# Optimization experiments

Hardware: AMD Instinct MI355X
Metric: run time of the kernel (lower is better)

The kernel has to match this reference:

```python
import jax, jax.numpy as jnp
import numpy as np

C = 256
CQK = C // 8  # query/key channels from Conv2d(in_dim, in_dim//8, 1)


def _cross_attn(x, y, qw, qb, kw, kb, vw, vb, gamma):
    # x, y: [B, C, H, W]; 1x1 convs are channel matmuls
    B, Cc, H, W = x.shape
    N = H * W
    xf = x.reshape(B, Cc, N)
    yf = y.reshape(B, Cc, N)
    q = jnp.einsum('oc,bcn->bno', qw, xf) + qb  # [B, N, CQK]
    k = jnp.einsum('oc,bcn->bon', kw, yf) + kb[:, None]  # [B, CQK, N]
    energy = jnp.einsum('bnc,bcm->bnm', q, k)  # [B, N, N]
    attn = jax.nn.softmax(energy, axis=2)
    v = jnp.einsum('oc,bcn->bon', vw, yf) + vb[:, None]  # [B, C, N]
    out = jnp.einsum('bcm,bnm->bcn', v, attn)  # value @ attention^T
    out = out.reshape(B, Cc, H, W)
    return gamma * out + x


def setup_inputs() -> dict:
    key = jax.random.key(0)
    ks = jax.random.split(key, 16)
    B, H, W = 4, 64, 64
    s = 1.0 / np.sqrt(C)
    d = {
        'x': jax.random.normal(ks[0], (B, C, H, W), jnp.float32),
        'y': jax.random.normal(ks[1], (B, C, H, W), jnp.float32),
        'z': jax.random.normal(ks[2], (B, C, H, W), jnp.float32),
        'q1_w': jax.random.normal(ks[3], (CQK, C), jnp.float32) * s,
        'q1_b': jax.random.normal(ks[4], (CQK,), jnp.float32) * s,
        'k1_w': jax.random.normal(ks[5], (CQK, C), jnp.float32) * s,
        'k1_b': jax.random.normal(ks[6], (CQK,), jnp.float32) * s,
        'v1_w': jax.random.normal(ks[7], (C, C), jnp.float32) * s,
        'v1_b': jax.random.normal(ks[8], (C,), jnp.float32) * s,
        'gamma1': jax.random.normal(ks[9], (1,), jnp.float32) * 0.1,
        'q2_w': jax.random.normal(ks[10], (CQK, C), jnp.float32) * s,
        'q2_b': jax.random.normal(ks[11], (CQK,), jnp.float32) * s,
        'k2_w': jax.random.normal(ks[12], (CQK, C), jnp.float32) * s,
        'k2_b': jax.random.normal(ks[13], (CQK,), jnp.float32) * s,
        'v2_w': jax.random.normal(ks[14], (C, C), jnp.float32) * s,
        'v2_b': jax.random.normal(ks[15], (C,), jnp.float32) * s,
        'gamma2': jax.random.normal(jax.random.fold_in(key, 99), (1,), jnp.float32) * 0.1,
    }
    return d


def reference(x, y, z, q1_w, q1_b, k1_w, k1_b, v1_w, v1_b, gamma1,
              q2_w, q2_b, k2_w, k2_b, v2_w, v2_b, gamma2):
    out1 = _cross_attn(x, y, q1_w, q1_b, k1_w, k1_b, v1_w, v1_b, gamma1)
    out2 = _cross_attn(out1, z, q2_w, q2_b, k2_w, k2_b, v2_w, v2_b, gamma2)
    return out2
```

## Files before the change

### kernel.cpp

```cpp
#include <hip/hip_runtime.h>
#include <hip/hip_bf16.h>

#define NSEQ 4096
#define CDIM 256
#define CQKD 32
#define LOG2E 1.4426950408889634f

typedef float v4f __attribute__((ext_vector_type(4)));
typedef float v16f __attribute__((ext_vector_type(16)));
typedef short v8s __attribute__((ext_vector_type(8)));
typedef unsigned long long u64;

__device__ __forceinline__ float exp2_(float x) {
#if __has_builtin(__builtin_amdgcn_exp2f)
  return __builtin_amdgcn_exp2f(x);
#else
  float r;
  __asm__("v_exp_f32 %0, %1" : "=v"(r) : "v"(x));
  return r;
#endif
}

__device__ __forceinline__ unsigned short f2bf(float x) {
  unsigned u = __builtin_bit_cast(unsigned, x);
  unsigned r = (u + 0x7FFFu + ((u >> 16) & 1u)) >> 16;
  return (unsigned short)r;
}
__device__ __forceinline__ float bf2f(unsigned short s) {
  unsigned u = ((unsigned)s) << 16;
  return __builtin_bit_cast(float, u);
}
__device__ __forceinline__ unsigned int pack_bf16(float a, float b) {
#if __has_builtin(__builtin_amdgcn_cvt_pk_bf16_f32)
  typedef __bf16 v2bf __attribute__((ext_vector_type(2)));
  v2bf r = __builtin_amdgcn_cvt_pk_bf16_f32(a, b);
  return __builtin_bit_cast(unsigned int, r);
#else
  return ((unsigned)f2bf(b) << 16) | (unsigned)f2bf(a);
#endif
}

__device__ __forceinline__ unsigned char f2e4m3(float x) {
  unsigned u = __builtin_bit_cast(unsigned, x);
  unsigned s = (u >> 24) & 0x80u;
  unsigned au = u & 0x7fffffffu;
  if (au > 0x43e00000u) return (unsigned char)(s | 0x7eu);
  if (au < 0x3c800000u) {
    float ax = __builtin_bit_cast(float, au);
    int q = (int)(ax * 512.0f + 0.5f);
    if (q > 7) q = 7;
    return (unsigned char)(s | (unsigned)q);
  }
  int e = (int)((au >> 23) & 0xffu) - 127 + 7;
  unsigned m = au & 0x7fffffu;
  unsigned mr = m + 0x7ffffu + ((m >> 20) & 1u);
  if (mr >= 0x800000u) { mr -= 0x800000u; e += 1; if (e >= 16) return (unsigned char)(s | 0x7e); }
  return (unsigned char)(s | ((unsigned)e << 3) | (mr >> 20));
}
__device__ __forceinline__ unsigned int pack4_fp8(float a, float b, float c, float d) {
#if __has_builtin(__builtin_amdgcn_cvt_pk_fp8_f32)
  int v = 0;
  v = __builtin_amdgcn_cvt_pk_fp8_f32(a, b, v, false);
  v = __builtin_amdgcn_cvt_pk_fp8_f32(c, d, v, true);
  return (unsigned int)v;
#else
  return (unsigned)f2e4m3(a) | ((unsigned)f2e4m3(b) << 8) |
         ((unsigned)f2e4m3(c) << 16) | ((unsigned)f2e4m3(d) << 24);
#endif
}

__device__ __forceinline__ void barrier_lds() {
  __asm__ __volatile__("s_waitcnt lgkmcnt(0)\n\ts_barrier" ::: "memory");
}

__global__ __launch_bounds__(256) void convw_kernel(
    const float* __restrict__ q1w, const float* __restrict__ k1w,
    const float* __restrict__ k2w, const float* __restrict__ q2w,
    const float* __restrict__ v1w, const float* __restrict__ v2w,
    unsigned short* __restrict__ W) {
  const int s = blockIdx.x * 256 + threadIdx.x;
  const float* src;
  int o, ch0;
  size_t obase;
  float scale = 1.0f;
  if (s < 3072) {
    const int wsel = s >> 10, r = s & 1023;
    src = wsel == 0 ? q1w : (wsel == 1 ? k1w : k2w);
    const int ot = r >> 9, cb = (r >> 6) & 7, lane = r & 63;
    o = ot * 16 + (lane & 15);
    ch0 = cb * 32 + ((lane >> 4) & 3) * 8;
    obase = (size_t)wsel * 8192 + (size_t)r * 8;
  } else if (s < 19456) {
    const int s2 = s - 3072, which = s2 >> 13, r = s2 & 8191;
    src = which == 0 ? v1w : v2w;
    const int ot = r >> 9, cb = (r >> 6) & 7, lane = r & 63;
    o = ot * 16 + (lane & 15);
    ch0 = cb * 32 + ((lane >> 4) & 3) * 8;
    obase = 32768 + (size_t)which * 65536 + (size_t)r * 8;
  } else {
    const int r = s - 19456;
    src = q2w;
    const int lane = r & 63;
    o = lane & 31;
    ch0 = (r >> 6) * 16 + (lane >> 5) * 8;
    obase = 24576 + (size_t)r * 8;
    scale = LOG2E;
  }
#pragma unroll
  for (int j = 0; j < 8; ++j)
    W[obase + j] = f2bf(src[o * CDIM + ch0 + j] * scale);
}

__global__ __launch_bounds__(256) void prep_kernel(
    const float* __restrict__ x, const float* __restrict__ y,
    const float* __restrict__ z, const unsigned short* __restrict__ Wbf,
    const float* __restrict__ q1b, const float* __restrict__ k1b,
    const float* __restrict__ k2b, const float* __restrict__ v1b,
    const float* __restrict__ v2b, unsigned short* __restrict__ Q1,
    unsigned short* __restrict__ K1, unsigned short* __restrict__ K2,
    unsigned char* __restrict__ V1, unsigned char* __restrict__ V2) {
  __shared__ unsigned short t[256][72];
  __shared__ unsigned short Kt[64][40];
  const int src = blockIdx.z;
  const float* in = src == 0 ? x : (src == 1 ? y : z);
  const int b = blockIdx.y;
  const int n0 = blockIdx.x * 64;
  const int tid = threadIdx.x, lane = tid & 63, w = tid >> 6;
  const int quad = lane >> 4, r15 = lane & 15, l31 = lane & 31, lh = lane >> 5;
  const float* ip = in + (size_t)(b * CDIM) * NSEQ + n0;
  {
    const int chb = tid >> 4, c4 = (tid & 15) * 4;
#pragma unroll
    for (int p = 0; p < 16; ++p) {
      const int ch = p * 16 + chb;
      float4 v = *(const float4*)(ip + (size_t)ch * NSEQ + c4);
      uint2 pk;
      pk.x = pack_bf16(v.x, v.y);
      pk.y = pack_bf16(v.z, v.w);
      *(uint2*)&t[ch][c4] = pk;
    }
  }
  __syncthreads();
  v8s af[8];
#pragma unroll
  for (int cb = 0; cb < 8; ++cb) {
    union { unsigned short e[8]; v8s v; } u;
#pragma unroll
    for (int j = 0; j < 8; ++j) u.e[j] = t[cb * 32 + quad * 8 + j][w * 16 + r15];
    af[cb] = u.v;
  }
  const int nt = blockIdx.x * 4 + w;
  const unsigned short* Wqk = Wbf + src * 8192;
  v4f a0 = {0.f, 0.f, 0.f, 0.f}, a1 = a0;
#pragma unroll
  for (int cb = 0; cb < 8; ++cb) {
    v8s b0 = *(const v8s*)(Wqk + (size_t)cb * 512 + lane * 8);
    v8s b1 = *(const v8s*)(Wqk + (size_t)(8 + cb) * 512 + lane * 8);
    a0 = __builtin_amdgcn_mfma_f32_16x16x32_bf16(af[cb], b0, a0, 0, 0, 0);
    a1 = __builtin_amdgcn_mfma_f32_16x16x32_bf16(af[cb], b1, a1, 0, 0, 0);
  }
  if (src == 0) {
#pragma unroll
    for (int r = 0; r < 4; ++r) {
      Q1[((size_t)b * NSEQ + nt * 16 + quad * 4 + r) * CQKD + r15] =
          f2bf((a0[r] + q1b[r15]) * LOG2E);
      Q1[((size_t)b * NSEQ + nt * 16 + quad * 4 + r) * CQKD + 16 + r15] =
          f2bf((a1[r] + q1b[16 + r15]) * LOG2E);
    }
    return;
  }
  const float* kbias = src == 1 ? k1b : k2b;
#pragma unroll
  for (int r = 0; r < 4; ++r) {
    Kt[w * 16 + quad * 4 + r][r15] = f2bf(a0[r] + kbias[r15]);
    Kt[w * 16 + quad * 4 + r][16 + r15] = f2bf(a1[r] + kbias[16 + r15]);
  }
  const unsigned short* Wv = Wbf + 32768 + (src - 1) * 65536;
  const float* vbias = src == 1 ? v1b : v2b;
  v4f vacc[16];
#pragma unroll
  for (int ot = 0; ot < 16; ++ot) vacc[ot] = (v4f){0.f, 0.f, 0.f, 0.f};
#pragma unroll
  for (int cb = 0; cb < 8; ++cb) {
    const v8s afc = af[cb];
#pragma unroll
    for (int ot = 0; ot < 16; ++ot) {
      v8s bf = *(const v8s*)(Wv + (size_t)(ot * 8 + cb) * 512 + lane * 8);
      vacc[ot] = __builtin_amdgcn_mfma_f32_16x16x32_bf16(afc, bf, vacc[ot], 0, 0, 0);
    }
  }
  __syncthreads();
  unsigned char* Vt8 = (unsigned char*)t;
#pragma unroll
  for (int ot = 0; ot < 16; ++ot) {
    const int ch = ot * 16 + r15;
    const float bv = vbias[ch];
    *(unsigned int*)&Vt8[(size_t)ch * 72 + w * 16 + quad * 4] =
        pack4_fp8(vacc[ot][0] + bv, vacc[ot][1] + bv, vacc[ot][2] + bv, vacc[ot][3] + bv);
  }
  {
    unsigned short* Kout = (src == 1 ? K1 : K2) + (size_t)b * (NSEQ / 16) * 512;
    *(v8s*)(Kout + ((size_t)nt * 64 + lane) * 8) = *(const v8s*)&Kt[w * 16 + r15][quad * 8];
  }
  __syncthreads();
  unsigned char* Vout = (src == 1 ? V1 : V2) + (size_t)b * (NSEQ / 16) * 8 * 512;
#pragma unroll
  for (int chb = 0; chb < 8; ++chb)
    *(u64*)(Vout + (((size_t)nt * 8 + chb) * 64 + lane) * 8) =
        *(const u64*)&Vt8[(size_t)(chb * 32 + l31) * 72 + w * 16 + lh * 8];
}


__device__ __forceinline__ void max_pass(
    const unsigned short* __restrict__ Kp, const v8s qf[4], int w, int lane,
    float (*lbuf)[64], float m[4]) {
  const v4f vzero4 = {0.f, 0.f, 0.f, 0.f};
  const int r15 = lane & 15;
  const unsigned short* Kl = Kp + (size_t)w * 512 + lane * 8;
  v8s kA = *(const v8s*)(Kl);
#pragma unroll
  for (int qt = 0; qt < 4; ++qt) m[qt] = -3.0e38f;
  for (int kt = 0; kt < 32; ++kt) {
    v8s kB = *(const v8s*)(Kl + (size_t)((kt + 1) & 31) * 4096);
#pragma unroll
    for (int qt = 0; qt < 4; ++qt) {
      v4f st = __builtin_amdgcn_mfma_f32_16x16x32_bf16(kA, qf[qt], vzero4, 0, 0, 0);
      m[qt] = fmaxf(m[qt], fmaxf(fmaxf(st[0], st[1]), fmaxf(st[2], st[3])));
    }
    kA = kB;
  }
#pragma unroll
  for (int qt = 0; qt < 4; ++qt) {
    m[qt] = fmaxf(m[qt], __shfl_xor(m[qt], 16));
    m[qt] = fmaxf(m[qt], __shfl_xor(m[qt], 32));
  }
  if (lane < 16) {
#pragma unroll
    for (int qt = 0; qt < 4; ++qt) lbuf[w][qt * 16 + lane] = m[qt];
  }
  __syncthreads();
#pragma unroll
  for (int qt = 0; qt < 4; ++qt) {
    float mm = lbuf[0][qt * 16 + r15];
#pragma unroll
    for (int ww = 1; ww < 8; ++ww) mm = fmaxf(mm, lbuf[ww][qt * 16 + r15]);
    m[qt] = mm;
  }
  __syncthreads();
}

__device__ __forceinline__ void attn_tile(
    const unsigned short* __restrict__ Kl, const unsigned char* __restrict__ Vl,
    unsigned char* __restrict__ P, const v8s qf[4], const float m[4], int w, int lane,
    int pbuf, int tn, const v8s kfu, const u64* vfu, v8s& kfn, u64* vfn,
    v16f acc[2], float lsum[4]) {
  const v4f vzero4 = {0.f, 0.f, 0.f, 0.f};
  const int quad = (lane >> 4) & 3, r15 = lane & 15;
  const int l31 = lane & 31, lh = lane >> 5;
  kfn = *(const v8s*)(Kl + (size_t)tn * 4096);
#pragma unroll
  for (int s = 0; s < 8; ++s)
    vfn[s] = *(const u64*)(Vl + (size_t)tn * 32768 + s * 4096);
  unsigned char* pw = P + pbuf * 8704 + w * 16 + quad * 4;
#pragma unroll
  for (int qt = 0; qt < 4; ++qt) {
    v4f st = __builtin_amdgcn_mfma_f32_16x16x32_bf16(kfu, qf[qt], vzero4, 0, 0, 0);
    float e0 = exp2_(st[0] - m[qt]), e1 = exp2_(st[1] - m[qt]);
    float e2 = exp2_(st[2] - m[qt]), e3 = exp2_(st[3] - m[qt]);
    lsum[qt] += (e0 + e1) + (e2 + e3);
    *(unsigned int*)(pw + (size_t)(qt * 16 + r15) * 136) = pack4_fp8(e0, e1, e2, e3);
  }
  barrier_lds();
  const unsigned char* pb = P + pbuf * 8704;
#pragma unroll
  for (int s = 0; s < 8; ++s) {
    long pf0 = (long)*(const u64*)(pb + (size_t)l31 * 136 + s * 16 + lh * 8);
    long pf1 = (long)*(const u64*)(pb + (size_t)(32 + l31) * 136 + s * 16 + lh * 8);
    acc[0] = __builtin_amdgcn_mfma_f32_32x32x16_fp8_fp8((long)vfu[s], pf0, acc[0], 0, 0, 0);
    acc[1] = __builtin_amdgcn_mfma_f32_32x32x16_fp8_fp8((long)vfu[s], pf1, acc[1], 0, 0, 0);
  }
}

__device__ __forceinline__ void attn_loop(
    const unsigned short* __restrict__ Kp, const unsigned char* __restrict__ Vp,
    unsigned char* __restrict__ P, const v8s qf[4], const float m[4], int w, int lane,
    v16f acc[2], float lsum[4]) {
  const unsigned short* Kl = Kp + (size_t)w * 512 + lane * 8;
  const unsigned char* Vl = Vp + (size_t)w * 512 + lane * 8;
  v8s kA, kB;
  u64 vA[8], vB[8];
  kA = *(const v8s*)(Kl);
#pragma unroll
  for (int s = 0; s < 8; ++s) vA[s] = *(const u64*)(Vl + (size_t)s * 4096);
  for (int kt = 0; kt < 32; kt += 2) {
    attn_tile(Kl, Vl, P, qf, m, w, lane, 0, (kt + 1) & 31, kA, vA, kB, vB, acc, lsum);
    attn_tile(Kl, Vl, P, qf, m, w, lane, 1, (kt + 2) & 31, kB, vB, kA, vA, acc, lsum);
  }
}

__global__ __launch_bounds__(512, 2) void fused_attn_kernel(
    const unsigned short* __restrict__ Q1g, const unsigned short* __restrict__ K1g,
    const unsigned char* __restrict__ V1g, const unsigned short* __restrict__ K2g,
    const unsigned char* __restrict__ V2g, const unsigned short* __restrict__ W2g,
    const float* __restrict__ x, const float* __restrict__ q2b,
    const float* __restrict__ g1p, const float* __restrict__ g2p,
    float* __restrict__ outp) {
  __shared__ __align__(16) unsigned char P[2 * 8704];
  __shared__ __align__(16) unsigned short out1T[64 * 264];
  __shared__ __align__(16) unsigned short q2s[64 * 32];
  __shared__ float lbuf[8][64];

  const int tid = threadIdx.x;
  const int lane = tid & 63;
  const int w = tid >> 6;
  const int quad = lane >> 4;
  const int r15 = lane & 15;
  const int l31 = lane & 31, lh = lane >> 5;
  const int b = blockIdx.x & 3;
  const int n0 = (blockIdx.x >> 2) * 64;

  const float g1 = g1p[0];
  const float g2 = g2p[0];

  const unsigned short* Qp  = Q1g + (size_t)b * NSEQ * CQKD;
  const unsigned short* K1p = K1g + (size_t)b * (NSEQ / 16) * 512;
  const unsigned short* K2p = K2g + (size_t)b * (NSEQ / 16) * 512;
  const unsigned char* V1p  = V1g + (size_t)b * (NSEQ / 16) * 8 * 512;
  const unsigned char* V2p  = V2g + (size_t)b * (NSEQ / 16) * 8 * 512;

  v8s qf[4];
#pragma unroll
  for (int qt = 0; qt < 4; ++qt)
    qf[qt] = *(const v8s*)(Qp + (n0 + qt * 16 + r15) * CQKD + quad * 8);

  v16f acc[2];
  float lsum[4] = {0.f, 0.f, 0.f, 0.f};
  float m[4];
  acc[0] = (v16f)(0.f); acc[1] = (v16f)(0.f);

  max_pass(K1p, qf, w, lane, lbuf, m);
  attn_loop(K1p, V1p, P, qf, m, w, lane, acc, lsum);
#pragma unroll
  for (int qt = 0; qt < 4; ++qt) {
    lsum[qt] += __shfl_xor(lsum[qt], 16);
    lsum[qt] += __shfl_xor(lsum[qt], 32);
  }
  __syncthreads();
  if (lane < 16) {
#pragma unroll
    for (int qt = 0; qt < 4; ++qt) lbuf[w][qt * 16 + lane] = lsum[qt];
  }
  __syncthreads();
  float rinv[2];
#pragma unroll
  for (int qh = 0; qh < 2; ++qh) {
    const int q = qh * 32 + l31;
    float d = 0.f;
#pragma unroll
    for (int ww = 0; ww < 8; ++ww) d += lbuf[ww][q];
    rinv[qh] = 1.0f / d;
  }
#pragma unroll
  for (int qh = 0; qh < 2; ++qh) {
    const int q = qh * 32 + l31;
#pragma unroll
    for (int rg = 0; rg < 4; ++rg) {
      const int c = w * 32 + 8 * rg + 4 * lh;
      float o0 = g1 * (acc[qh][rg * 4 + 0] * rinv[qh]) + x[((size_t)b * CDIM + c + 0) * NSEQ + n0 + q];
      float o1 = g1 * (acc[qh][rg * 4 + 1] * rinv[qh]) + x[((size_t)b * CDIM + c + 1) * NSEQ + n0 + q];
      float o2 = g1 * (acc[qh][rg * 4 + 2] * rinv[qh]) + x[((size_t)b * CDIM + c + 2) * NSEQ + n0 + q];
      float o3 = g1 * (acc[qh][rg * 4 + 3] * rinv[qh]) + x[((size_t)b * CDIM + c + 3) * NSEQ + n0 + q];
      uint2 pk;
      pk.x = pack_bf16(o0, o1);
      pk.y = pack_bf16(o2, o3);
      *(uint2*)(out1T + (size_t)q * 264 + c) = pk;
    }
  }
  __syncthreads();

  if (w < 2) {
    const int qh = w;
    v16f qacc = (v16f)(0.f);
#pragma unroll
    for (int s = 0; s < 16; ++s) {
      v8s af = *(const v8s*)(W2g + (size_t)(s * 64 + lane) * 8);
      v8s bf = *(const v8s*)(out1T + (size_t)(qh * 32 + l31) * 264 + s * 16 + lh * 8);
      qacc = __builtin_amdgcn_mfma_f32_32x32x16_bf16(af, bf, qacc, 0, 0, 0);
    }
#pragma unroll
    for (int rg = 0; rg < 4; ++rg) {
      const int o = 8 * rg + 4 * lh;
      uint2 pk;
      pk.x = pack_bf16(qacc[rg * 4 + 0] + q2b[o + 0] * LOG2E, qacc[rg * 4 + 1] + q2b[o + 1] * LOG2E);
      pk.y = pack_bf16(qacc[rg * 4 + 2] + q2b[o + 2] * LOG2E, qacc[rg * 4 + 3] + q2b[o + 3] * LOG2E);
      *(uint2*)(q2s + (size_t)(qh * 32 + l31) * 32 + o) = pk;
    }
  }
  __syncthreads();

#pragma unroll
  for (int qt = 0; qt < 4; ++qt)
    qf[qt] = *(const v8s*)(q2s + (qt * 16 + r15) * 32 + quad * 8);
  acc[0] = (v16f)(0.f); acc[1] = (v16f)(0.f);
#pragma unroll
  for (int qt = 0; qt < 4; ++qt) lsum[qt] = 0.f;
  max_pass(K2p, qf, w, lane, lbuf, m);
  attn_loop(K2p, V2p, P, qf, m, w, lane, acc, lsum);
#pragma unroll
  for (int qt = 0; qt < 4; ++qt) {
    lsum[qt] += __shfl_xor(lsum[qt], 16);
    lsum[qt] += __shfl_xor(lsum[qt], 32);
  }
  __syncthreads();
  if (lane < 16) {
#pragma unroll
    for (int qt = 0; qt < 4; ++qt) lbuf[w][qt * 16 + lane] = lsum[qt];
  }
  __syncthreads();
#pragma unroll
  for (int qh = 0; qh < 2; ++qh) {
    const int q = qh * 32 + l31;
    float d = 0.f;
#pragma unroll
    for (int ww = 0; ww < 8; ++ww) d += lbuf[ww][q];
    rinv[qh] = 1.0f / d;
  }
#pragma unroll
  for (int qh = 0; qh < 2; ++qh) {
    const int q = qh * 32 + l31;
#pragma unroll
    for (int rg = 0; rg < 4; ++rg) {
      const int c = w * 32 + 8 * rg + 4 * lh;
#pragma unroll
      for (int i = 0; i < 4; ++i) {
        float res = bf2f(out1T[(size_t)q * 264 + c + i]);
        outp[((size_t)b * CDIM + c + i) * NSEQ + n0 + q] =
            g2 * (acc[qh][rg * 4 + i] * rinv[qh]) + res;
      }
    }
  }
}

extern "C" void kernel_launch(void* const* d_in, const int* in_sizes, int n_in,
                              void* d_out, int out_size, void* d_ws, size_t ws_size,
                              hipStream_t stream) {
  const float* x   = (const float*)d_in[0];
  const float* y   = (const float*)d_in[1];
  const float* z   = (const float*)d_in[2];
  const float* q1w = (const float*)d_in[3];
  const float* q1b = (const float*)d_in[4];
  const float* k1w = (const float*)d_in[5];
  const float* k1b = (const float*)d_in[6];
  const float* v1w = (const float*)d_in[7];
  const float* v1b = (const float*)d_in[8];
  const float* g1  = (const float*)d_in[9];
  const float* q2w = (const float*)d_in[10];
  const float* q2b = (const float*)d_in[11];
  const float* k2w = (const float*)d_in[12];
  const float* k2b = (const float*)d_in[13];
  const float* v2w = (const float*)d_in[14];
  const float* v2b = (const float*)d_in[15];
  const float* g2  = (const float*)d_in[16];
  char* ws = (char*)d_ws;
  unsigned short* Wbf = (unsigned short*)(ws);
  unsigned short* Q1  = (unsigned short*)(ws + 327680);
  unsigned short* K1  = (unsigned short*)(ws + 1376256);
  unsigned short* K2  = (unsigned short*)(ws + 2424832);
  unsigned char*  V1  = (unsigned char*)(ws + 3473408);
  unsigned char*  V2  = (unsigned char*)(ws + 7667712);
  float* outp = (float*)d_out;

  convw_kernel<<<dim3(80), 256, 0, stream>>>(q1w, k1w, k2w, q2w, v1w, v2w, Wbf);
  prep_kernel<<<dim3(64, 4, 3), 256, 0, stream>>>(x, y, z, Wbf, q1b, k1b, k2b, v1b,
                                                  v2b, Q1, K1, K2, V1, V2);
  fused_attn_kernel<<<dim3(256), 512, 0, stream>>>(Q1, K1, V1, K2, V2, Wbf + 24576, x,
                                                   q2b, g1, g2, outp);
}
```

Baseline: 222.1 us.

## Replace two-pass softmax with online split-K attention and shuffle-based P exchange

Drops the separate max pass over K and switches each attention stage to online softmax, rescaling lazily only when the running max grows by more than a threshold. The key dimension is split across four waves per query group of 32, and partial accumulators are merged at the end through LDS with the max/sum correction. The probability tile is rebuilt in registers with cross-lane shuffles instead of an LDS write, barrier and read. Each wave now holds eight 32x32 fp32 accumulators plus prefetched V fragments. That adds a lot of register pressure under the 512x2 launch bounds and a serial three-round LDS reduction.

```diff
diff --git a/kernel.cpp b/kernel.cpp
--- a/kernel.cpp
+++ b/kernel.cpp
@@ -67,10 +67,6 @@
   return (unsigned)f2e4m3(a) | ((unsigned)f2e4m3(b) << 8) |
          ((unsigned)f2e4m3(c) << 16) | ((unsigned)f2e4m3(d) << 24);
 #endif
-}
-
-__device__ __forceinline__ void barrier_lds() {
-  __asm__ __volatile__("s_waitcnt lgkmcnt(0)\n\ts_barrier" ::: "memory");
 }
 
 __global__ __launch_bounds__(256) void convw_kernel(
@@ -211,91 +207,67 @@
 }
 
 
-__device__ __forceinline__ void max_pass(
-    const unsigned short* __restrict__ Kp, const v8s qf[4], int w, int lane,
-    float (*lbuf)[64], float m[4]) {
-  const v4f vzero4 = {0.f, 0.f, 0.f, 0.f};
-  const int r15 = lane & 15;
-  const unsigned short* Kl = Kp + (size_t)w * 512 + lane * 8;
-  v8s kA = *(const v8s*)(Kl);
-#pragma unroll
-  for (int qt = 0; qt < 4; ++qt) m[qt] = -3.0e38f;
-  for (int kt = 0; kt < 32; ++kt) {
-    v8s kB = *(const v8s*)(Kl + (size_t)((kt + 1) & 31) * 4096);
-#pragma unroll
-    for (int qt = 0; qt < 4; ++qt) {
-      v4f st = __builtin_amdgcn_mfma_f32_16x16x32_bf16(kA, qf[qt], vzero4, 0, 0, 0);
-      m[qt] = fmaxf(m[qt], fmaxf(fmaxf(st[0], st[1]), fmaxf(st[2], st[3])));
-    }
-    kA = kB;
-  }
-#pragma unroll
-  for (int qt = 0; qt < 4; ++qt) {
-    m[qt] = fmaxf(m[qt], __shfl_xor(m[qt], 16));
-    m[qt] = fmaxf(m[qt], __shfl_xor(m[qt], 32));
-  }
-  if (lane < 16) {
-#pragma unroll
-    for (int qt = 0; qt < 4; ++qt) lbuf[w][qt * 16 + lane] = m[qt];
-  }
-  __syncthreads();
-#pragma unroll
-  for (int qt = 0; qt < 4; ++qt) {
-    float mm = lbuf[0][qt * 16 + r15];
-#pragma unroll
-    for (int ww = 1; ww < 8; ++ww) mm = fmaxf(mm, lbuf[ww][qt * 16 + r15]);
-    m[qt] = mm;
-  }
-  __syncthreads();
-}
-
-__device__ __forceinline__ void attn_tile(
-    const unsigned short* __restrict__ Kl, const unsigned char* __restrict__ Vl,
-    unsigned char* __restrict__ P, const v8s qf[4], const float m[4], int w, int lane,
-    int pbuf, int tn, const v8s kfu, const u64* vfu, v8s& kfn, u64* vfn,
-    v16f acc[2], float lsum[4]) {
-  const v4f vzero4 = {0.f, 0.f, 0.f, 0.f};
-  const int quad = (lane >> 4) & 3, r15 = lane & 15;
+__device__ __forceinline__ void attn_ks(
+    const unsigned short* __restrict__ Kp, const unsigned char* __restrict__ Vp,
+    const v8s qfA, const v8s qfB, int ks, int lane,
+    v16f acc[8], float& m, float& lsum) {
   const int l31 = lane & 31, lh = lane >> 5;
-  kfn = *(const v8s*)(Kl + (size_t)tn * 4096);
-#pragma unroll
-  for (int s = 0; s < 8; ++s)
-    vfn[s] = *(const u64*)(Vl + (size_t)tn * 32768 + s * 4096);
-  unsigned char* pw = P + pbuf * 8704 + w * 16 + quad * 4;
-#pragma unroll
-  for (int qt = 0; qt < 4; ++qt) {
-    v4f st = __builtin_amdgcn_mfma_f32_16x16x32_bf16(kfu, qf[qt], vzero4, 0, 0, 0);
-    float e0 = exp2_(st[0] - m[qt]), e1 = exp2_(st[1] - m[qt]);
-    float e2 = exp2_(st[2] - m[qt]), e3 = exp2_(st[3] - m[qt]);
-    lsum[qt] += (e0 + e1) + (e2 + e3);
-    *(unsigned int*)(pw + (size_t)(qt * 16 + r15) * 136) = pack4_fp8(e0, e1, e2, e3);
-  }
-  barrier_lds();
-  const unsigned char* pb = P + pbuf * 8704;
-#pragma unroll
-  for (int s = 0; s < 8; ++s) {
-    long pf0 = (long)*(const u64*)(pb + (size_t)l31 * 136 + s * 16 + lh * 8);
-    long pf1 = (long)*(const u64*)(pb + (size_t)(32 + l31) * 136 + s * 16 + lh * 8);
-    acc[0] = __builtin_amdgcn_mfma_f32_32x32x16_fp8_fp8((long)vfu[s], pf0, acc[0], 0, 0, 0);
-    acc[1] = __builtin_amdgcn_mfma_f32_32x32x16_fp8_fp8((long)vfu[s], pf1, acc[1], 0, 0, 0);
-  }
-}
-
-__device__ __forceinline__ void attn_loop(
-    const unsigned short* __restrict__ Kp, const unsigned char* __restrict__ Vp,
-    unsigned char* __restrict__ P, const v8s qf[4], const float m[4], int w, int lane,
-    v16f acc[2], float lsum[4]) {
-  const unsigned short* Kl = Kp + (size_t)w * 512 + lane * 8;
-  const unsigned char* Vl = Vp + (size_t)w * 512 + lane * 8;
-  v8s kA, kB;
-  u64 vA[8], vB[8];
-  kA = *(const v8s*)(Kl);
-#pragma unroll
-  for (int s = 0; s < 8; ++s) vA[s] = *(const u64*)(Vl + (size_t)s * 4096);
-  for (int kt = 0; kt < 32; kt += 2) {
-    attn_tile(Kl, Vl, P, qf, m, w, lane, 0, (kt + 1) & 31, kA, vA, kB, vB, acc, lsum);
-    attn_tile(Kl, Vl, P, qf, m, w, lane, 1, (kt + 2) & 31, kB, vB, kA, vA, acc, lsum);
-  }
+  const char* Kb = (const char*)Kp + (size_t)ks * 65536 + (size_t)(l31 >> 4) * 1024 +
+                   (size_t)lh * 256 + (size_t)(l31 & 15) * 16;
+  const char* Vb = (const char*)Vp + (size_t)ks * 262144 + (size_t)lane * 8;
+  m = -3.0e38f;
+  lsum = 0.f;
+  v8s kA = *(const v8s*)(Kb);
+  v8s kB = *(const v8s*)(Kb + 512);
+#pragma unroll 1
+  for (int t = 0; t < 32; ++t) {
+    u64 v0[8], v1[8];
+#pragma unroll
+    for (int s = 0; s < 8; ++s) v0[s] = *(const u64*)(Vb + (size_t)t * 8192 + s * 512);
+#pragma unroll
+    for (int s = 0; s < 8; ++s) v1[s] = *(const u64*)(Vb + (size_t)t * 8192 + 4096 + s * 512);
+    v16f st = (v16f)(0.f);
+    st = __builtin_amdgcn_mfma_f32_32x32x16_bf16(kA, qfA, st, 0, 0, 0);
+    st = __builtin_amdgcn_mfma_f32_32x32x16_bf16(kB, qfB, st, 0, 0, 0);
+    if (t < 31) {
+      kA = *(const v8s*)(Kb + (size_t)(t + 1) * 2048);
+      kB = *(const v8s*)(Kb + (size_t)(t + 1) * 2048 + 512);
+    }
+    float tmax = st[0];
+#pragma unroll
+    for (int g = 1; g < 16; ++g) tmax = fmaxf(tmax, st[g]);
+    tmax = fmaxf(tmax, __shfl_xor(tmax, 32));
+    if (__any(tmax > m + 8.0f)) {
+      float mn = fmaxf(m, tmax);
+      float sc = exp2_(m - mn);
+#pragma unroll
+      for (int s = 0; s < 8; ++s) acc[s] *= sc;
+      lsum *= sc;
+      m = mn;
+    }
+    float esum = 0.f;
+    unsigned pw[4];
+#pragma unroll
+    for (int h = 0; h < 4; ++h) {
+      float e0 = exp2_(st[4 * h + 0] - m), e1 = exp2_(st[4 * h + 1] - m);
+      float e2 = exp2_(st[4 * h + 2] - m), e3 = exp2_(st[4 * h + 3] - m);
+      esum += (e0 + e1) + (e2 + e3);
+      pw[h] = pack4_fp8(e0, e1, e2, e3);
+    }
+    lsum += esum;
+    unsigned X0 = (unsigned)__shfl_xor((int)pw[0], 32);
+    unsigned X1 = (unsigned)__shfl_xor((int)pw[1], 32);
+    unsigned X2 = (unsigned)__shfl_xor((int)pw[2], 32);
+    unsigned X3 = (unsigned)__shfl_xor((int)pw[3], 32);
+    u64 fA = lh ? ((u64)X1 | ((u64)pw[1] << 32)) : ((u64)pw[0] | ((u64)X0 << 32));
+    u64 fB = lh ? ((u64)X3 | ((u64)pw[3] << 32)) : ((u64)pw[2] | ((u64)X2 << 32));
+#pragma unroll
+    for (int s = 0; s < 8; ++s) {
+      acc[s] = __builtin_amdgcn_mfma_f32_32x32x16_fp8_fp8((long)v0[s], (long)fA, acc[s], 0, 0, 0);
+      acc[s] = __builtin_amdgcn_mfma_f32_32x32x16_fp8_fp8((long)v1[s], (long)fB, acc[s], 0, 0, 0);
+    }
+  }
+  lsum += __shfl_xor(lsum, 32);
 }
 
 __global__ __launch_bounds__(512, 2) void fused_attn_kernel(
@@ -305,19 +277,21 @@
     const float* __restrict__ x, const float* __restrict__ q2b,
     const float* __restrict__ g1p, const float* __restrict__ g2p,
     float* __restrict__ outp) {
-  __shared__ __align__(16) unsigned char P[2 * 8704];
+  __shared__ float cb[2][256][32];
   __shared__ __align__(16) unsigned short out1T[64 * 264];
   __shared__ __align__(16) unsigned short q2s[64 * 32];
-  __shared__ float lbuf[8][64];
+  __shared__ float mbuf[8][32];
+  __shared__ float sbuf[8][32];
 
   const int tid = threadIdx.x;
   const int lane = tid & 63;
   const int w = tid >> 6;
-  const int quad = lane >> 4;
-  const int r15 = lane & 15;
+  const int qg = w >> 2;
+  const int ks = w & 3;
   const int l31 = lane & 31, lh = lane >> 5;
   const int b = blockIdx.x & 3;
   const int n0 = (blockIdx.x >> 2) * 64;
+  const int q = qg * 32 + l31;
 
   const float g1 = g1p[0];
   const float g2 = g2p[0];
@@ -328,52 +302,61 @@
   const unsigned char* V1p  = V1g + (size_t)b * (NSEQ / 16) * 8 * 512;
   const unsigned char* V2p  = V2g + (size_t)b * (NSEQ / 16) * 8 * 512;
 
-  v8s qf[4];
-#pragma unroll
-  for (int qt = 0; qt < 4; ++qt)
-    qf[qt] = *(const v8s*)(Qp + (n0 + qt * 16 + r15) * CQKD + quad * 8);
-
-  v16f acc[2];
-  float lsum[4] = {0.f, 0.f, 0.f, 0.f};
-  float m[4];
-  acc[0] = (v16f)(0.f); acc[1] = (v16f)(0.f);
-
-  max_pass(K1p, qf, w, lane, lbuf, m);
-  attn_loop(K1p, V1p, P, qf, m, w, lane, acc, lsum);
-#pragma unroll
-  for (int qt = 0; qt < 4; ++qt) {
-    lsum[qt] += __shfl_xor(lsum[qt], 16);
-    lsum[qt] += __shfl_xor(lsum[qt], 32);
-  }
-  __syncthreads();
-  if (lane < 16) {
-#pragma unroll
-    for (int qt = 0; qt < 4; ++qt) lbuf[w][qt * 16 + lane] = lsum[qt];
-  }
-  __syncthreads();
-  float rinv[2];
-#pragma unroll
-  for (int qh = 0; qh < 2; ++qh) {
-    const int q = qh * 32 + l31;
-    float d = 0.f;
-#pragma unroll
-    for (int ww = 0; ww < 8; ++ww) d += lbuf[ww][q];
-    rinv[qh] = 1.0f / d;
-  }
-#pragma unroll
-  for (int qh = 0; qh < 2; ++qh) {
-    const int q = qh * 32 + l31;
-#pragma unroll
-    for (int rg = 0; rg < 4; ++rg) {
-      const int c = w * 32 + 8 * rg + 4 * lh;
-      float o0 = g1 * (acc[qh][rg * 4 + 0] * rinv[qh]) + x[((size_t)b * CDIM + c + 0) * NSEQ + n0 + q];
-      float o1 = g1 * (acc[qh][rg * 4 + 1] * rinv[qh]) + x[((size_t)b * CDIM + c + 1) * NSEQ + n0 + q];
-      float o2 = g1 * (acc[qh][rg * 4 + 2] * rinv[qh]) + x[((size_t)b * CDIM + c + 2) * NSEQ + n0 + q];
-      float o3 = g1 * (acc[qh][rg * 4 + 3] * rinv[qh]) + x[((size_t)b * CDIM + c + 3) * NSEQ + n0 + q];
-      uint2 pk;
-      pk.x = pack_bf16(o0, o1);
-      pk.y = pack_bf16(o2, o3);
-      *(uint2*)(out1T + (size_t)q * 264 + c) = pk;
+  v16f acc[8];
+#pragma unroll
+  for (int s = 0; s < 8; ++s) acc[s] = (v16f)(0.f);
+  float m, lsum;
+
+  {
+    v8s qfA = *(const v8s*)(Qp + (size_t)(n0 + q) * CQKD + lh * 8);
+    v8s qfB = *(const v8s*)(Qp + (size_t)(n0 + q) * CQKD + 16 + lh * 8);
+    attn_ks(K1p, V1p, qfA, qfB, ks, lane, acc, m, lsum);
+  }
+  mbuf[w][l31] = m;
+  sbuf[w][l31] = lsum;
+  __syncthreads();
+  float mstar = mbuf[qg * 4 + 0][l31];
+#pragma unroll
+  for (int k = 1; k < 4; ++k) mstar = fmaxf(mstar, mbuf[qg * 4 + k][l31]);
+  float L = 0.f;
+#pragma unroll
+  for (int k = 0; k < 4; ++k) L += sbuf[qg * 4 + k][l31] * exp2_(mbuf[qg * 4 + k][l31] - mstar);
+  {
+    float sc = exp2_(m - mstar);
+#pragma unroll
+    for (int s = 0; s < 8; ++s) acc[s] *= sc;
+  }
+#pragma unroll 1
+  for (int r = 1; r < 4; ++r) {
+    if (ks == r) {
+#pragma unroll
+      for (int s = 0; s < 8; ++s)
+#pragma unroll
+        for (int g = 0; g < 16; ++g)
+          cb[qg][s * 32 + (g & 3) + 8 * (g >> 2) + 4 * lh][l31] = acc[s][g];
+    }
+    __syncthreads();
+    if (ks == 0) {
+#pragma unroll
+      for (int s = 0; s < 8; ++s)
+#pragma unroll
+        for (int g = 0; g < 16; ++g)
+          acc[s][g] += cb[qg][s * 32 + (g & 3) + 8 * (g >> 2) + 4 * lh][l31];
+    }
+    __syncthreads();
+  }
+  if (ks == 0) {
+    const float rinv = 1.0f / L;
+    const float* xb = x + (size_t)b * CDIM * NSEQ + n0 + q;
+#pragma unroll
+    for (int s = 0; s < 8; ++s) {
+#pragma unroll
+      for (int j = 0; j < 8; ++j) {
+        const int ch = s * 32 + ((2 * j) & 3) + 8 * (j >> 1) + 4 * lh;
+        float o0 = g1 * (acc[s][2 * j] * rinv) + xb[(size_t)ch * NSEQ];
+        float o1 = g1 * (acc[s][2 * j + 1] * rinv) + xb[(size_t)(ch + 1) * NSEQ];
+        *(unsigned*)(&out1T[(size_t)q * 264 + ch]) = pack_bf16(o0, o1);
+      }
     }
   }
   __syncthreads();
@@ -399,43 +382,57 @@
   __syncthreads();
 
 #pragma unroll
-  for (int qt = 0; qt < 4; ++qt)
-    qf[qt] = *(const v8s*)(q2s + (qt * 16 + r15) * 32 + quad * 8);
-  acc[0] = (v16f)(0.f); acc[1] = (v16f)(0.f);
-#pragma unroll
-  for (int qt = 0; qt < 4; ++qt) lsum[qt] = 0.f;
-  max_pass(K2p, qf, w, lane, lbuf, m);
-  attn_loop(K2p, V2p, P, qf, m, w, lane, acc, lsum);
-#pragma unroll
-  for (int qt = 0; qt < 4; ++qt) {
-    lsum[qt] += __shfl_xor(lsum[qt], 16);
-    lsum[qt] += __shfl_xor(lsum[qt], 32);
-  }
-  __syncthreads();
-  if (lane < 16) {
-#pragma unroll
-    for (int qt = 0; qt < 4; ++qt) lbuf[w][qt * 16 + lane] = lsum[qt];
-  }
-  __syncthreads();
-#pragma unroll
-  for (int qh = 0; qh < 2; ++qh) {
-    const int q = qh * 32 + l31;
-    float d = 0.f;
-#pragma unroll
-    for (int ww = 0; ww < 8; ++ww) d += lbuf[ww][q];
-    rinv[qh] = 1.0f / d;
-  }
-#pragma unroll
-  for (int qh = 0; qh < 2; ++qh) {
-    const int q = qh * 32 + l31;
-#pragma unroll
-    for (int rg = 0; rg < 4; ++rg) {
-      const int c = w * 32 + 8 * rg + 4 * lh;
-#pragma unroll
-      for (int i = 0; i < 4; ++i) {
-        float res = bf2f(out1T[(size_t)q * 264 + c + i]);
-        outp[((size_t)b * CDIM + c + i) * NSEQ + n0 + q] =
-            g2 * (acc[qh][rg * 4 + i] * rinv[qh]) + res;
+  for (int s = 0; s < 8; ++s) acc[s] = (v16f)(0.f);
+  {
+    v8s qfA = *(const v8s*)(q2s + (size_t)q * 32 + lh * 8);
+    v8s qfB = *(const v8s*)(q2s + (size_t)q * 32 + 16 + lh * 8);
+    attn_ks(K2p, V2p, qfA, qfB, ks, lane, acc, m, lsum);
+  }
+  mbuf[w][l31] = m;
+  sbuf[w][l31] = lsum;
+  __syncthreads();
+  mstar = mbuf[qg * 4 + 0][l31];
+#pragma unroll
+  for (int k = 1; k < 4; ++k) mstar = fmaxf(mstar, mbuf[qg * 4 + k][l31]);
+  L = 0.f;
+#pragma unroll
+  for (int k = 0; k < 4; ++k) L += sbuf[qg * 4 + k][l31] * exp2_(mbuf[qg * 4 + k][l31] - mstar);
+  {
+    float sc = exp2_(m - mstar);
+#pragma unroll
+    for (int s = 0; s < 8; ++s) acc[s] *= sc;
+  }
+#pragma unroll 1
+  for (int r = 1; r < 4; ++r) {
+    if (ks == r) {
+#pragma unroll
+      for (int s = 0; s < 8; ++s)
+#pragma unroll
+        for (int g = 0; g < 16; ++g)
+          cb[qg][s * 32 + (g & 3) + 8 * (g >> 2) + 4 * lh][l31] = acc[s][g];
+    }
+    __syncthreads();
+    if (ks == 0) {
+#pragma unroll
+      for (int s = 0; s < 8; ++s)
+#pragma unroll
+        for (int g = 0; g < 16; ++g)
+          acc[s][g] += cb[qg][s * 32 + (g & 3) + 8 * (g >> 2) + 4 * lh][l31];
+    }
+    __syncthreads();
+  }
+  if (ks == 0) {
+    const float rinv = 1.0f / L;
+    float* ob = outp + (size_t)b * CDIM * NSEQ + n0 + q;
+#pragma unroll
+    for (int s = 0; s < 8; ++s) {
+#pragma unroll
+      for (int j = 0; j < 8; ++j) {
+        const int ch = s * 32 + ((2 * j) & 3) + 8 * (j >> 1) + 4 * lh;
+        float r0 = bf2f(out1T[(size_t)q * 264 + ch]);
+        float r1 = bf2f(out1T[(size_t)q * 264 + ch + 1]);
+        ob[(size_t)ch * NSEQ] = g2 * (acc[s][2 * j] * rinv) + r0;
+        ob[(size_t)(ch + 1) * NSEQ] = g2 * (acc[s][2 * j + 1] * rinv) + r1;
       }
     }
   }
```

After: 248.7 us. 12.0% more time.

## Software-pipeline attention loop: overlap next tile's scores with current PV MFMAs

Applied to the files above, without the earlier changes.

Restructures the attention inner loop so each step computes the QK scores and fp8 P tile for tile t+1 while running the PV MFMAs on tile t from the other P buffer. This cuts one barrier per tile and lets exp/score work overlap the matrix work. V loads are issued after the PV MFMAs, and the max pass gets deeper K prefetch with unroll 2. Register pressure rises and the prefetch distances have to line up with the double-buffered P.

```diff
diff --git a/kernel.cpp b/kernel.cpp
--- a/kernel.cpp
+++ b/kernel.cpp
@@ -218,16 +218,19 @@
   const int r15 = lane & 15;
   const unsigned short* Kl = Kp + (size_t)w * 512 + lane * 8;
   v8s kA = *(const v8s*)(Kl);
+  v8s kB = *(const v8s*)(Kl + 4096);
 #pragma unroll
   for (int qt = 0; qt < 4; ++qt) m[qt] = -3.0e38f;
+#pragma unroll 2
   for (int kt = 0; kt < 32; ++kt) {
-    v8s kB = *(const v8s*)(Kl + (size_t)((kt + 1) & 31) * 4096);
+    v8s kC = *(const v8s*)(Kl + (size_t)((kt + 2) & 31) * 4096);
 #pragma unroll
     for (int qt = 0; qt < 4; ++qt) {
       v4f st = __builtin_amdgcn_mfma_f32_16x16x32_bf16(kA, qf[qt], vzero4, 0, 0, 0);
       m[qt] = fmaxf(m[qt], fmaxf(fmaxf(st[0], st[1]), fmaxf(st[2], st[3])));
     }
     kA = kB;
+    kB = kC;
   }
 #pragma unroll
   for (int qt = 0; qt < 4; ++qt) {
@@ -249,42 +252,46 @@
   __syncthreads();
 }
 
-__device__ __forceinline__ void attn_tile(
+__device__ __forceinline__ void attn_step(
     const unsigned short* __restrict__ Kl, const unsigned char* __restrict__ Vl,
     unsigned char* __restrict__ P, const v8s qf[4], const float m[4], int w, int lane,
-    int pbuf, int tn, const v8s kfu, const u64* vfu, v8s& kfn, u64* vfn,
+    bool doS, int pbufW, int pbufR, int tpre, const v8s kS, v8s& kOut, u64 vUse[8],
     v16f acc[2], float lsum[4]) {
   const v4f vzero4 = {0.f, 0.f, 0.f, 0.f};
   const int quad = (lane >> 4) & 3, r15 = lane & 15;
   const int l31 = lane & 31, lh = lane >> 5;
-  kfn = *(const v8s*)(Kl + (size_t)tn * 4096);
-#pragma unroll
-  for (int s = 0; s < 8; ++s)
-    vfn[s] = *(const u64*)(Vl + (size_t)tn * 32768 + s * 4096);
-  unsigned char* pw = P + pbuf * 8704 + w * 16 + quad * 4;
-#pragma unroll
-  for (int qt = 0; qt < 4; ++qt) {
-    v4f st = __builtin_amdgcn_mfma_f32_16x16x32_bf16(kfu, qf[qt], vzero4, 0, 0, 0);
-    float e0 = exp2_(st[0] - m[qt]), e1 = exp2_(st[1] - m[qt]);
-    float e2 = exp2_(st[2] - m[qt]), e3 = exp2_(st[3] - m[qt]);
-    lsum[qt] += (e0 + e1) + (e2 + e3);
-    *(unsigned int*)(pw + (size_t)(qt * 16 + r15) * 136) = pack4_fp8(e0, e1, e2, e3);
-  }
-  barrier_lds();
-  const unsigned char* pb = P + pbuf * 8704;
+  kOut = *(const v8s*)(Kl + (size_t)tpre * 4096);
+  if (doS) {
+    unsigned char* pw = P + pbufW * 8704 + w * 16 + quad * 4;
+#pragma unroll
+    for (int qt = 0; qt < 4; ++qt) {
+      v4f st = __builtin_amdgcn_mfma_f32_16x16x32_bf16(kS, qf[qt], vzero4, 0, 0, 0);
+      float e0 = exp2_(st[0] - m[qt]), e1 = exp2_(st[1] - m[qt]);
+      float e2 = exp2_(st[2] - m[qt]), e3 = exp2_(st[3] - m[qt]);
+      lsum[qt] += (e0 + e1) + (e2 + e3);
+      *(unsigned int*)(pw + (size_t)(qt * 16 + r15) * 136) = pack4_fp8(e0, e1, e2, e3);
+    }
+  }
+  const unsigned char* pb = P + pbufR * 8704;
 #pragma unroll
   for (int s = 0; s < 8; ++s) {
     long pf0 = (long)*(const u64*)(pb + (size_t)l31 * 136 + s * 16 + lh * 8);
     long pf1 = (long)*(const u64*)(pb + (size_t)(32 + l31) * 136 + s * 16 + lh * 8);
-    acc[0] = __builtin_amdgcn_mfma_f32_32x32x16_fp8_fp8((long)vfu[s], pf0, acc[0], 0, 0, 0);
-    acc[1] = __builtin_amdgcn_mfma_f32_32x32x16_fp8_fp8((long)vfu[s], pf1, acc[1], 0, 0, 0);
-  }
+    acc[0] = __builtin_amdgcn_mfma_f32_32x32x16_fp8_fp8((long)vUse[s], pf0, acc[0], 0, 0, 0);
+    acc[1] = __builtin_amdgcn_mfma_f32_32x32x16_fp8_fp8((long)vUse[s], pf1, acc[1], 0, 0, 0);
+  }
+#pragma unroll
+  for (int s = 0; s < 8; ++s)
+    vUse[s] = *(const u64*)(Vl + (size_t)tpre * 32768 + s * 4096);
+  barrier_lds();
 }
 
 __device__ __forceinline__ void attn_loop(
     const unsigned short* __restrict__ Kp, const unsigned char* __restrict__ Vp,
     unsigned char* __restrict__ P, const v8s qf[4], const float m[4], int w, int lane,
     v16f acc[2], float lsum[4]) {
+  const v4f vzero4 = {0.f, 0.f, 0.f, 0.f};
+  const int quad = lane >> 4, r15 = lane & 15;
   const unsigned short* Kl = Kp + (size_t)w * 512 + lane * 8;
   const unsigned char* Vl = Vp + (size_t)w * 512 + lane * 8;
   v8s kA, kB;
@@ -292,9 +299,24 @@
   kA = *(const v8s*)(Kl);
 #pragma unroll
   for (int s = 0; s < 8; ++s) vA[s] = *(const u64*)(Vl + (size_t)s * 4096);
-  for (int kt = 0; kt < 32; kt += 2) {
-    attn_tile(Kl, Vl, P, qf, m, w, lane, 0, (kt + 1) & 31, kA, vA, kB, vB, acc, lsum);
-    attn_tile(Kl, Vl, P, qf, m, w, lane, 1, (kt + 2) & 31, kB, vB, kA, vA, acc, lsum);
+  kB = *(const v8s*)(Kl + 4096);
+#pragma unroll
+  for (int s = 0; s < 8; ++s) vB[s] = *(const u64*)(Vl + 32768 + s * 4096);
+  {
+    unsigned char* pw = P + w * 16 + quad * 4;
+#pragma unroll
+    for (int qt = 0; qt < 4; ++qt) {
+      v4f st = __builtin_amdgcn_mfma_f32_16x16x32_bf16(kA, qf[qt], vzero4, 0, 0, 0);
+      float e0 = exp2_(st[0] - m[qt]), e1 = exp2_(st[1] - m[qt]);
+      float e2 = exp2_(st[2] - m[qt]), e3 = exp2_(st[3] - m[qt]);
+      lsum[qt] += (e0 + e1) + (e2 + e3);
+      *(unsigned int*)(pw + (size_t)(qt * 16 + r15) * 136) = pack4_fp8(e0, e1, e2, e3);
+    }
+  }
+  barrier_lds();
+  for (int t = 0; t < 32; t += 2) {
+    attn_step(Kl, Vl, P, qf, m, w, lane, true, 1, 0, (t + 2) & 31, kB, kA, vA, acc, lsum);
+    attn_step(Kl, Vl, P, qf, m, w, lane, t != 30, 0, 1, (t + 3) & 31, kA, kB, vB, acc, lsum);
   }
 }
 
```

New measurement: 230.3 us. 1.04x slower.

## Warp-specialize attention into score/softmax producer and PV-MFMA consumer waves

Applied to the files above, without the earlier changes.

Raises the block from 8 to 16 waves. The max pass now spreads its key tiles across all 16 waves. In the main loop, waves 0-7 compute QK scores, exp and fp8 packing into a double-buffered shared P tile, while waves 8-15 load V and run the PV fp8 MFMAs one tile behind, with a block barrier each step. This is meant to overlap the exp/softmax work with the PV matrix work. It costs a block-wide barrier per tile and more register pressure under the tighter launch bounds, and the producer/consumer balance is uneven.

```diff
diff --git a/kernel.cpp b/kernel.cpp
--- a/kernel.cpp
+++ b/kernel.cpp
@@ -211,23 +211,26 @@
 }
 
 
-__device__ __forceinline__ void max_pass(
+__device__ __forceinline__ void max_pass16(
     const unsigned short* __restrict__ Kp, const v8s qf[4], int w, int lane,
     float (*lbuf)[64], float m[4]) {
   const v4f vzero4 = {0.f, 0.f, 0.f, 0.f};
   const int r15 = lane & 15;
   const unsigned short* Kl = Kp + (size_t)w * 512 + lane * 8;
   v8s kA = *(const v8s*)(Kl);
+  v8s kB = *(const v8s*)(Kl + 8192);
 #pragma unroll
   for (int qt = 0; qt < 4; ++qt) m[qt] = -3.0e38f;
-  for (int kt = 0; kt < 32; ++kt) {
-    v8s kB = *(const v8s*)(Kl + (size_t)((kt + 1) & 31) * 4096);
+#pragma unroll 2
+  for (int kt = 0; kt < 16; ++kt) {
+    v8s kC = *(const v8s*)(Kl + (size_t)((kt + 2) & 15) * 8192);
 #pragma unroll
     for (int qt = 0; qt < 4; ++qt) {
       v4f st = __builtin_amdgcn_mfma_f32_16x16x32_bf16(kA, qf[qt], vzero4, 0, 0, 0);
       m[qt] = fmaxf(m[qt], fmaxf(fmaxf(st[0], st[1]), fmaxf(st[2], st[3])));
     }
     kA = kB;
+    kB = kC;
   }
 #pragma unroll
   for (int qt = 0; qt < 4; ++qt) {
@@ -243,62 +246,74 @@
   for (int qt = 0; qt < 4; ++qt) {
     float mm = lbuf[0][qt * 16 + r15];
 #pragma unroll
-    for (int ww = 1; ww < 8; ++ww) mm = fmaxf(mm, lbuf[ww][qt * 16 + r15]);
+    for (int ww = 1; ww < 16; ++ww) mm = fmaxf(mm, lbuf[ww][qt * 16 + r15]);
     m[qt] = mm;
   }
   __syncthreads();
 }
 
-__device__ __forceinline__ void attn_tile(
-    const unsigned short* __restrict__ Kl, const unsigned char* __restrict__ Vl,
-    unsigned char* __restrict__ P, const v8s qf[4], const float m[4], int w, int lane,
-    int pbuf, int tn, const v8s kfu, const u64* vfu, v8s& kfn, u64* vfn,
-    v16f acc[2], float lsum[4]) {
+__device__ __forceinline__ void s_phase(
+    unsigned char* __restrict__ P, int pbuf, const v8s kf, const v8s qf[4],
+    const float m[4], int w, int lane, float lsum[4]) {
   const v4f vzero4 = {0.f, 0.f, 0.f, 0.f};
-  const int quad = (lane >> 4) & 3, r15 = lane & 15;
-  const int l31 = lane & 31, lh = lane >> 5;
-  kfn = *(const v8s*)(Kl + (size_t)tn * 4096);
-#pragma unroll
-  for (int s = 0; s < 8; ++s)
-    vfn[s] = *(const u64*)(Vl + (size_t)tn * 32768 + s * 4096);
+  const int quad = lane >> 4, r15 = lane & 15;
   unsigned char* pw = P + pbuf * 8704 + w * 16 + quad * 4;
 #pragma unroll
   for (int qt = 0; qt < 4; ++qt) {
-    v4f st = __builtin_amdgcn_mfma_f32_16x16x32_bf16(kfu, qf[qt], vzero4, 0, 0, 0);
+    v4f st = __builtin_amdgcn_mfma_f32_16x16x32_bf16(kf, qf[qt], vzero4, 0, 0, 0);
     float e0 = exp2_(st[0] - m[qt]), e1 = exp2_(st[1] - m[qt]);
     float e2 = exp2_(st[2] - m[qt]), e3 = exp2_(st[3] - m[qt]);
     lsum[qt] += (e0 + e1) + (e2 + e3);
     *(unsigned int*)(pw + (size_t)(qt * 16 + r15) * 136) = pack4_fp8(e0, e1, e2, e3);
   }
-  barrier_lds();
-  const unsigned char* pb = P + pbuf * 8704;
-#pragma unroll
-  for (int s = 0; s < 8; ++s) {
-    long pf0 = (long)*(const u64*)(pb + (size_t)l31 * 136 + s * 16 + lh * 8);
-    long pf1 = (long)*(const u64*)(pb + (size_t)(32 + l31) * 136 + s * 16 + lh * 8);
-    acc[0] = __builtin_amdgcn_mfma_f32_32x32x16_fp8_fp8((long)vfu[s], pf0, acc[0], 0, 0, 0);
-    acc[1] = __builtin_amdgcn_mfma_f32_32x32x16_fp8_fp8((long)vfu[s], pf1, acc[1], 0, 0, 0);
-  }
 }
 
 __device__ __forceinline__ void attn_loop(
     const unsigned short* __restrict__ Kp, const unsigned char* __restrict__ Vp,
     unsigned char* __restrict__ P, const v8s qf[4], const float m[4], int w, int lane,
     v16f acc[2], float lsum[4]) {
-  const unsigned short* Kl = Kp + (size_t)w * 512 + lane * 8;
-  const unsigned char* Vl = Vp + (size_t)w * 512 + lane * 8;
-  v8s kA, kB;
-  u64 vA[8], vB[8];
-  kA = *(const v8s*)(Kl);
-#pragma unroll
-  for (int s = 0; s < 8; ++s) vA[s] = *(const u64*)(Vl + (size_t)s * 4096);
-  for (int kt = 0; kt < 32; kt += 2) {
-    attn_tile(Kl, Vl, P, qf, m, w, lane, 0, (kt + 1) & 31, kA, vA, kB, vB, acc, lsum);
-    attn_tile(Kl, Vl, P, qf, m, w, lane, 1, (kt + 2) & 31, kB, vB, kA, vA, acc, lsum);
-  }
-}
-
-__global__ __launch_bounds__(512, 2) void fused_attn_kernel(
+  if (w < 8) {
+    const unsigned short* Kl = Kp + (size_t)w * 512 + lane * 8;
+    v8s kA = *(const v8s*)(Kl);
+    v8s kB = *(const v8s*)(Kl + 4096);
+    s_phase(P, 0, kA, qf, m, w, lane, lsum);
+    barrier_lds();
+#pragma unroll 2
+    for (int t = 0; t < 32; ++t) {
+      v8s kC = *(const v8s*)(Kl + (size_t)((t + 2) & 31) * 4096);
+      if (t < 31) s_phase(P, (t + 1) & 1, kB, qf, m, w, lane, lsum);
+      kA = kB;
+      kB = kC;
+      barrier_lds();
+    }
+  } else {
+    const int l31 = lane & 31, lh = lane >> 5;
+    const unsigned char* Vl = Vp + (size_t)(w - 8) * 512 + lane * 8;
+    u64 vA[8], vB[8];
+#pragma unroll
+    for (int s = 0; s < 8; ++s) vA[s] = *(const u64*)(Vl + (size_t)s * 4096);
+    barrier_lds();
+#pragma unroll 2
+    for (int t = 0; t < 32; ++t) {
+#pragma unroll
+      for (int s = 0; s < 8; ++s)
+        vB[s] = *(const u64*)(Vl + (size_t)((t + 1) & 31) * 32768 + s * 4096);
+      const unsigned char* pb = P + (t & 1) * 8704;
+#pragma unroll
+      for (int s = 0; s < 8; ++s) {
+        long pf0 = (long)*(const u64*)(pb + (size_t)l31 * 136 + s * 16 + lh * 8);
+        long pf1 = (long)*(const u64*)(pb + (size_t)(32 + l31) * 136 + s * 16 + lh * 8);
+        acc[0] = __builtin_amdgcn_mfma_f32_32x32x16_fp8_fp8((long)vA[s], pf0, acc[0], 0, 0, 0);
+        acc[1] = __builtin_amdgcn_mfma_f32_32x32x16_fp8_fp8((long)vA[s], pf1, acc[1], 0, 0, 0);
+      }
+#pragma unroll
+      for (int s = 0; s < 8; ++s) vA[s] = vB[s];
+      barrier_lds();
+    }
+  }
+}
+
+__global__ __launch_bounds__(1024, 4) void fused_attn_kernel(
     const unsigned short* __restrict__ Q1g, const unsigned short* __restrict__ K1g,
     const unsigned char* __restrict__ V1g, const unsigned short* __restrict__ K2g,
     const unsigned char* __restrict__ V2g, const unsigned short* __restrict__ W2g,
@@ -308,7 +323,7 @@
   __shared__ __align__(16) unsigned char P[2 * 8704];
   __shared__ __align__(16) unsigned short out1T[64 * 264];
   __shared__ __align__(16) unsigned short q2s[64 * 32];
-  __shared__ float lbuf[8][64];
+  __shared__ float lbuf[16][64];
 
   const int tid = threadIdx.x;
   const int lane = tid & 63;
@@ -338,17 +353,18 @@
   float m[4];
   acc[0] = (v16f)(0.f); acc[1] = (v16f)(0.f);
 
-  max_pass(K1p, qf, w, lane, lbuf, m);
+  max_pass16(K1p, qf, w, lane, lbuf, m);
   attn_loop(K1p, V1p, P, qf, m, w, lane, acc, lsum);
-#pragma unroll
-  for (int qt = 0; qt < 4; ++qt) {
-    lsum[qt] += __shfl_xor(lsum[qt], 16);
-    lsum[qt] += __shfl_xor(lsum[qt], 32);
-  }
-  __syncthreads();
-  if (lane < 16) {
-#pragma unroll
-    for (int qt = 0; qt < 4; ++qt) lbuf[w][qt * 16 + lane] = lsum[qt];
+  if (w < 8) {
+#pragma unroll
+    for (int qt = 0; qt < 4; ++qt) {
+      lsum[qt] += __shfl_xor(lsum[qt], 16);
+      lsum[qt] += __shfl_xor(lsum[qt], 32);
+    }
+    if (lane < 16) {
+#pragma unroll
+      for (int qt = 0; qt < 4; ++qt) lbuf[w][qt * 16 + lane] = lsum[qt];
+    }
   }
   __syncthreads();
   float rinv[2];
@@ -360,20 +376,23 @@
     for (int ww = 0; ww < 8; ++ww) d += lbuf[ww][q];
     rinv[qh] = 1.0f / d;
   }
-#pragma unroll
-  for (int qh = 0; qh < 2; ++qh) {
-    const int q = qh * 32 + l31;
-#pragma unroll
-    for (int rg = 0; rg < 4; ++rg) {
-      const int c = w * 32 + 8 * rg + 4 * lh;
-      float o0 = g1 * (acc[qh][rg * 4 + 0] * rinv[qh]) + x[((size_t)b * CDIM + c + 0) * NSEQ + n0 + q];
-      float o1 = g1 * (acc[qh][rg * 4 + 1] * rinv[qh]) + x[((size_t)b * CDIM + c + 1) * NSEQ + n0 + q];
-      float o2 = g1 * (acc[qh][rg * 4 + 2] * rinv[qh]) + x[((size_t)b * CDIM + c + 2) * NSEQ + n0 + q];
-      float o3 = g1 * (acc[qh][rg * 4 + 3] * rinv[qh]) + x[((size_t)b * CDIM + c + 3) * NSEQ + n0 + q];
-      uint2 pk;
-      pk.x = pack_bf16(o0, o1);
-      pk.y = pack_bf16(o2, o3);
-      *(uint2*)(out1T + (size_t)q * 264 + c) = pk;
+  if (w >= 8) {
+    const int cw = (w - 8) * 32;
+#pragma unroll
+    for (int qh = 0; qh < 2; ++qh) {
+      const int q = qh * 32 + l31;
+#pragma unroll
+      for (int rg = 0; rg < 4; ++rg) {
+        const int c = cw + 8 * rg + 4 * lh;
+        float o0 = g1 * (acc[qh][rg * 4 + 0] * rinv[qh]) + x[((size_t)b * CDIM + c + 0) * NSEQ + n0 + q];
+        float o1 = g1 * (acc[qh][rg * 4 + 1] * rinv[qh]) + x[((size_t)b * CDIM + c + 1) * NSEQ + n0 + q];
+        float o2 = g1 * (acc[qh][rg * 4 + 2] * rinv[qh]) + x[((size_t)b * CDIM + c + 2) * NSEQ + n0 + q];
+        float o3 = g1 * (acc[qh][rg * 4 + 3] * rinv[qh]) + x[((size_t)b * CDIM + c + 3) * NSEQ + n0 + q];
+        uint2 pk;
+        pk.x = pack_bf16(o0, o1);
+        pk.y = pack_bf16(o2, o3);
+        *(uint2*)(out1T + (size_t)q * 264 + c) = pk;
+      }
     }
   }
   __syncthreads();
@@ -404,17 +423,18 @@
   acc[0] = (v16f)(0.f); acc[1] = (v16f)(0.f);
 #pragma unroll
   for (int qt = 0; qt < 4; ++qt) lsum[qt] = 0.f;
-  max_pass(K2p, qf, w, lane, lbuf, m);
+  max_pass16(K2p, qf, w, lane, lbuf, m);
   attn_loop(K2p, V2p, P, qf, m, w, lane, acc, lsum);
-#pragma unroll
-  for (int qt = 0; qt < 4; ++qt) {
-    lsum[qt] += __shfl_xor(lsum[qt], 16);
-    lsum[qt] += __shfl_xor(lsum[qt], 32);
-  }
-  __syncthreads();
-  if (lane < 16) {
-#pragma unroll
-    for (int qt = 0; qt < 4; ++qt) lbuf[w][qt * 16 + lane] = lsum[qt];
+  if (w < 8) {
+#pragma unroll
+    for (int qt = 0; qt < 4; ++qt) {
+      lsum[qt] += __shfl_xor(lsum[qt], 16);
+      lsum[qt] += __shfl_xor(lsum[qt], 32);
+    }
+    if (lane < 16) {
+#pragma unroll
+      for (int qt = 0; qt < 4; ++qt) lbuf[w][qt * 16 + lane] = lsum[qt];
+    }
   }
   __syncthreads();
 #pragma unroll
@@ -425,17 +445,20 @@
     for (int ww = 0; ww < 8; ++ww) d += lbuf[ww][q];
     rinv[qh] = 1.0f / d;
   }
-#pragma unroll
-  for (int qh = 0; qh < 2; ++qh) {
-    const int q = qh * 32 + l31;
-#pragma unroll
-    for (int rg = 0; rg < 4; ++rg) {
-      const int c = w * 32 + 8 * rg + 4 * lh;
-#pragma unroll
-      for (int i = 0; i < 4; ++i) {
-        float res = bf2f(out1T[(size_t)q * 264 + c + i]);
-        outp[((size_t)b * CDIM + c + i) * NSEQ + n0 + q] =
-            g2 * (acc[qh][rg * 4 + i] * rinv[qh]) + res;
+  if (w >= 8) {
+    const int cw = (w - 8) * 32;
+#pragma unroll
+    for (int qh = 0; qh < 2; ++qh) {
+      const int q = qh * 32 + l31;
+#pragma unroll
+      for (int rg = 0; rg < 4; ++rg) {
+        const int c = cw + 8 * rg + 4 * lh;
+#pragma unroll
+        for (int i = 0; i < 4; ++i) {
+          float res = bf2f(out1T[(size_t)q * 264 + c + i]);
+          outp[((size_t)b * CDIM + c + i) * NSEQ + n0 + q] =
+              g2 * (acc[qh][rg * 4 + i] * rinv[qh]) + res;
+        }
       }
     }
   }
@@ -473,6 +496,6 @@
   convw_kernel<<<dim3(80), 256, 0, stream>>>(q1w, k1w, k2w, q2w, v1w, v2w, Wbf);
   prep_kernel<<<dim3(64, 4, 3), 256, 0, stream>>>(x, y, z, Wbf, q1b, k1b, k2b, v1b,
                                                   v2b, Q1, K1, K2, V1, V2);
-  fused_attn_kernel<<<dim3(256), 512, 0, stream>>>(Q1, K1, V1, K2, V2, Wbf + 24576, x,
-                                                   q2b, g1, g2, outp);
-}
+  fused_attn_kernel<<<dim3(256), 1024, 0, stream>>>(Q1, K1, V1, K2, V2, Wbf + 24576, x,
+                                                    q2b, g1, g2, outp);
+}
```

Result: faster. 214.2 us (-3.6%).
